# Optimization experiments

Measured on AMD Instinct MI355X. Metric: run time of the kernel, lower is better.

Reference implementation:

```python
import jax, jax.numpy as jnp
import numpy as np

B, S, D_IN, D_OUT = 4, 2048, 1024, 1024

def setup_inputs() -> dict:
    key = jax.random.key(0)
    k1, k2, k3, k4 = jax.random.split(key, 4)
    s = 0.02
    return {
        "X": jax.random.normal(k1, (B, S, D_IN), dtype=jnp.float32),
        "Wq": jax.random.normal(k2, (D_OUT, D_IN), dtype=jnp.float32) * s,
        "Wk": jax.random.normal(k3, (D_OUT, D_IN), dtype=jnp.float32) * s,
        "Wv": jax.random.normal(k4, (D_OUT, D_IN), dtype=jnp.float32) * s,
    }

def reference(X, Wq, Wk, Wv):
    # nn.Linear: y = x @ W.T (no bias)
    q = jnp.einsum('bsd,ed->bse', X, Wq)  # [B,S,D_OUT]
    k = jnp.einsum('bsd,ed->bse', X, Wk)
    v = jnp.einsum('bsd,ed->bse', X, Wv)
    scores = jnp.einsum('bqe,bke->bqk', q, k)  # [B,S,S]
    n = X.shape[1]
    causal = jnp.triu(jnp.ones((n, n), dtype=bool), k=1)
    scores = jnp.where(causal[None], -jnp.inf, scores)
    scale = 1.0 / jnp.sqrt(jnp.asarray(k.shape[-1], dtype=scores.dtype))
    attn = jax.nn.softmax(scores * scale, axis=-1)
    return jnp.einsum('bqk,bke->bqe', attn, v)
```

## Files before the change

kernel.cpp:

```cpp
#include <hip/hip_runtime.h>
#include <cstdint>


typedef __attribute__((ext_vector_type(8))) __bf16 bf16x8;
typedef __attribute__((ext_vector_type(4))) float f32x4;

#define BK 64

__device__ __forceinline__ unsigned short f2bf(float f) {
  union { float f; unsigned u; } v; v.f = f;
  unsigned r = v.u + 0x7fffu + ((v.u >> 16) & 1u);
  return (unsigned short)(r >> 16);
}

__device__ __forceinline__ void gload_lds16(const void* g, void* l) {
  __builtin_amdgcn_global_load_lds(
      (const __attribute__((address_space(1))) void*)g,
      (__attribute__((address_space(3))) void*)l, 16, 0, 0);
}

__global__ __launch_bounds__(256)
void cvt_all(const float* __restrict__ X, const float* __restrict__ Wq,
             const float* __restrict__ Wk, const float* __restrict__ Wv,
             unsigned short* __restrict__ Xbf, unsigned short* __restrict__ Wall,
             float* __restrict__ L) {
  const int bid = blockIdx.x;
  if (bid >= 11264) {
    float4* p = (float4*)(L + (size_t)(bid - 11264) * 2048);
    p[threadIdx.x] = (float4){0.f, 0.f, 0.f, 0.f};
    p[threadIdx.x + 256] = (float4){0.f, 0.f, 0.f, 0.f};
    return;
  }
  const float* src;
  unsigned short* dst;
  int i;
  if (bid < 8192) {
    src = X; dst = Xbf; i = bid * 256 + threadIdx.x;
  } else {
    const int m = bid - 8192;
    const int sel = m >> 10;
    src = (sel == 0) ? Wq : (sel == 1) ? Wk : Wv;
    dst = Wall + (size_t)sel * 1048576;
    i = (m & 1023) * 256 + threadIdx.x;
  }
  float4 v = ((const float4*)src)[i];
  ushort4 o;
  o.x = f2bf(v.x); o.y = f2bf(v.y); o.z = f2bf(v.z); o.w = f2bf(v.w);
  ((ushort4*)dst)[i] = o;
}

__global__ __launch_bounds__(256, 3)
void gemm_qkv(const unsigned short* __restrict__ A,
              const unsigned short* __restrict__ Bm,
              unsigned short* __restrict__ Qb,
              unsigned short* __restrict__ Kb)
{
  const int NX = gridDim.x;
  const int lin = blockIdx.y * NX + blockIdx.x;
  const int chunk = (NX * 64) >> 3;
  const int swz = (lin & 7) * chunk + (lin >> 3);
  const int bx = swz % NX, by = swz / NX;

  __shared__ __align__(16) unsigned short As[128 * BK];
  __shared__ __align__(16) unsigned short Bs[128 * BK];

  const int tid = threadIdx.x;
  const int wave = tid >> 6, lane = tid & 63;
  const int wr = wave >> 1, wc = wave & 1;
  const int quad = lane >> 4, l16 = lane & 15;

  const unsigned rsub = wave * 8 + (lane >> 3);
  const unsigned csb = (unsigned)(((lane & 7) ^ ((lane >> 3) & 7)) * 16);

  unsigned offA[4], offB[4];
  #pragma unroll
  for (int s = 0; s < 4; ++s) {
    offA[s] = ((unsigned)(by * 128 + s * 32 + rsub) * 1024u) * 2u + csb;
    offB[s] = ((unsigned)(bx * 128 + s * 32 + rsub) * 1024u) * 2u + csb;
  }
  const char* Abase = (const char*)A;
  const char* Bbase = (const char*)Bm;

  f32x4 acc[4][4];
  #pragma unroll
  for (int i = 0; i < 4; ++i)
    #pragma unroll
    for (int j = 0; j < 4; ++j)
      acc[i][j] = (f32x4){0.f, 0.f, 0.f, 0.f};

  const int pq = (quad ^ (l16 & 7)) * 8;
  const int aOff = (wr * 64 + l16) * BK + pq;
  const int bOff = (wc * 64 + l16) * BK + pq;

  for (int k0 = 0; k0 < 1024; k0 += BK) {
    const unsigned kb = (unsigned)k0 * 2u;
    #pragma unroll
    for (int s = 0; s < 4; ++s) {
      gload_lds16(Abase + kb + offA[s], As + s * 2048 + wave * 512);
      gload_lds16(Bbase + kb + offB[s], Bs + s * 2048 + wave * 512);
    }
    __syncthreads();
    #pragma unroll
    for (int h = 0; h < 2; ++h) {
      const int hx = h * 32;
      bf16x8 af[4], bfr[4];
      #pragma unroll
      for (int i = 0; i < 4; ++i)
        af[i] = *(const bf16x8*)(As + ((aOff + i * 16 * BK) ^ hx));
      #pragma unroll
      for (int j = 0; j < 4; ++j)
        bfr[j] = *(const bf16x8*)(Bs + ((bOff + j * 16 * BK) ^ hx));
      #pragma unroll
      for (int i = 0; i < 4; ++i)
        #pragma unroll
        for (int j = 0; j < 4; ++j)
          acc[i][j] = __builtin_amdgcn_mfma_f32_16x16x32_bf16(af[i], bfr[j], acc[i][j], 0, 0, 0);
    }
    __syncthreads();
  }

  const int row0 = by * 128 + wr * 64 + quad * 4;
  const int col0 = bx * 128 + wc * 64 + l16;
  unsigned short* C = (bx < 8) ? Qb : Kb;
  const int col = (bx < 8) ? col0 : col0 - 1024;
  #pragma unroll
  for (int i = 0; i < 4; ++i)
    #pragma unroll
    for (int r = 0; r < 4; ++r) {
      const size_t rr = (size_t)(row0 + i * 16 + r) * 1024;
      #pragma unroll
      for (int j = 0; j < 4; ++j)
        C[rr + col + j * 16] = f2bf(acc[i][j][r]);
    }
}

__global__ __launch_bounds__(256, 3)
void gemm_sv(const unsigned short* __restrict__ Qb,
             const unsigned short* __restrict__ Kb,
             const unsigned short* __restrict__ Xbf,
             const unsigned short* __restrict__ Wall,
             unsigned short* __restrict__ S,
             float* __restrict__ L,
             unsigned short* __restrict__ Vt)
{
  const int lin = blockIdx.x;
  const int c = lin & 7;
  const int pos = lin >> 3;
  const bool isV = (pos < 128) && (pos & 1);

  int by, bxr, bz = 0;
  const unsigned short *Ab, *Bb;
  if (!isV) {
    const int s_loc = (pos < 128) ? (pos >> 1) : (64 + (pos - 128));
    const int sidx = c * 68 + s_loc;
    bz = sidx / 136;
    const int t = sidx - bz * 136;
    int byy = (int)((sqrtf(8.f * t + 1.f) - 1.f) * 0.5f);
    while ((byy + 1) * (byy + 2) / 2 <= t) ++byy;
    while (byy * (byy + 1) / 2 > t) --byy;
    by = byy;
    bxr = t - byy * (byy + 1) / 2;
    Ab = Qb + (size_t)bz * 2097152;
    Bb = Kb + (size_t)bz * 2097152;
  } else {
    const int v = c * 64 + (pos >> 1);
    by = v >> 3;
    bxr = v & 7;
    Ab = Xbf;
    Bb = Wall + 2 * 1048576;
  }

  __shared__ __align__(16) unsigned short As2[128 * BK];
  __shared__ __align__(16) unsigned short Bs2[128 * BK];

  const int tid = threadIdx.x;
  const int wave = tid >> 6, lane = tid & 63;
  const int wr = wave >> 1, wc = wave & 1;
  const int quad = lane >> 4, l16 = lane & 15;

  const unsigned rsub = wave * 8 + (lane >> 3);
  const unsigned csb = (unsigned)(((lane & 7) ^ ((lane >> 3) & 7)) * 16);

  unsigned offA[4], offB[4];
  #pragma unroll
  for (int s = 0; s < 4; ++s) {
    offA[s] = ((unsigned)(by * 128 + s * 32 + rsub) * 1024u) * 2u + csb;
    offB[s] = ((unsigned)(bxr * 128 + s * 32 + rsub) * 1024u) * 2u + csb;
  }
  const char* Abase = (const char*)Ab;
  const char* Bbase = (const char*)Bb;

  f32x4 acc[4][4];
  #pragma unroll
  for (int i = 0; i < 4; ++i)
    #pragma unroll
    for (int j = 0; j < 4; ++j)
      acc[i][j] = (f32x4){0.f, 0.f, 0.f, 0.f};

  const int pq = (quad ^ (l16 & 7)) * 8;
  const int aOff = (wr * 64 + l16) * BK + pq;
  const int bOff = (wc * 64 + l16) * BK + pq;

  for (int k0 = 0; k0 < 1024; k0 += BK) {
    const unsigned kb = (unsigned)k0 * 2u;
    #pragma unroll
    for (int s = 0; s < 4; ++s) {
      gload_lds16(Abase + kb + offA[s], As2 + s * 2048 + wave * 512);
      gload_lds16(Bbase + kb + offB[s], Bs2 + s * 2048 + wave * 512);
    }
    __syncthreads();
    #pragma unroll
    for (int h = 0; h < 2; ++h) {
      const int hx = h * 32;
      bf16x8 af[4], bfr[4];
      #pragma unroll
      for (int i = 0; i < 4; ++i)
        af[i] = *(const bf16x8*)(As2 + ((aOff + i * 16 * BK) ^ hx));
      #pragma unroll
      for (int j = 0; j < 4; ++j)
        bfr[j] = *(const bf16x8*)(Bs2 + ((bOff + j * 16 * BK) ^ hx));
      #pragma unroll
      for (int i = 0; i < 4; ++i)
        #pragma unroll
        for (int j = 0; j < 4; ++j)
          acc[i][j] = __builtin_amdgcn_mfma_f32_16x16x32_bf16(af[i], bfr[j], acc[i][j], 0, 0, 0);
    }
    __syncthreads();
  }

  const int row0 = by * 128 + wr * 64 + quad * 4;
  if (!isV) {
    const int col0 = bxr * 128 + wc * 64 + l16;
    float* Lb = L + (size_t)bz * 2048;
    unsigned short* C = S + (size_t)bz * 4194304;
    #pragma unroll
    for (int i = 0; i < 4; ++i)
      #pragma unroll
      for (int r = 0; r < 4; ++r) {
        const int grow = row0 + i * 16 + r;
        float ps = 0.f;
        #pragma unroll
        for (int j = 0; j < 4; ++j) {
          const int gcol = col0 + j * 16;
          float e = (gcol <= grow) ? __expf(acc[i][j][r] * 0.03125f) : 0.f;
          acc[i][j][r] = e;
          ps += e;
        }
        #pragma unroll
        for (int m = 8; m > 0; m >>= 1)
          ps += __shfl_xor(ps, m);
        if (l16 == 0) atomicAdd(&Lb[grow], ps);
        const size_t rr = (size_t)grow * 2048;
        #pragma unroll
        for (int j = 0; j < 4; ++j)
          C[rr + col0 + j * 16] = f2bf(acc[i][j][r]);
      }
  } else {
    const int b = row0 >> 11;
    const int s0 = row0 & 2047;
    unsigned short* Vb = Vt + (size_t)b * 2097152;
    const int e0 = bxr * 128 + wc * 64 + l16;
    #pragma unroll
    for (int j = 0; j < 4; ++j) {
      const size_t ee = (size_t)(e0 + j * 16) * 2048;
      #pragma unroll
      for (int i = 0; i < 4; ++i) {
        ushort4 o;
        o.x = f2bf(acc[i][j][0]); o.y = f2bf(acc[i][j][1]);
        o.z = f2bf(acc[i][j][2]); o.w = f2bf(acc[i][j][3]);
        *(ushort4*)(Vb + ee + s0 + i * 16) = o;
      }
    }
  }
}

__global__ __launch_bounds__(256, 3)
void gemm_pv(const unsigned short* __restrict__ P,
             const unsigned short* __restrict__ Vt,
             float* __restrict__ Out,
             const float* __restrict__ L)
{
  const int bx = blockIdx.x, by = 15 - blockIdx.y, bz = blockIdx.z;

  __shared__ __align__(16) unsigned short As2[128 * BK];
  __shared__ __align__(16) unsigned short Bs2[128 * BK];

  const int tid = threadIdx.x;
  const int wave = tid >> 6, lane = tid & 63;
  const int wr = wave >> 1, wc = wave & 1;
  const int quad = lane >> 4, l16 = lane & 15;

  const unsigned rsub = wave * 8 + (lane >> 3);
  const unsigned csb = (unsigned)(((lane & 7) ^ ((lane >> 3) & 7)) * 16);

  unsigned offA[4], offB[4];
  #pragma unroll
  for (int s = 0; s < 4; ++s) {
    offA[s] = ((unsigned)(by * 128 + s * 32 + rsub) * 2048u) * 2u + csb;
    offB[s] = ((unsigned)(bx * 128 + s * 32 + rsub) * 2048u) * 2u + csb;
  }
  const char* Abase = (const char*)(P + (size_t)bz * 4194304);
  const char* Bbase = (const char*)(Vt + (size_t)bz * 2097152);

  f32x4 acc[4][4];
  #pragma unroll
  for (int i = 0; i < 4; ++i)
    #pragma unroll
    for (int j = 0; j < 4; ++j)
      acc[i][j] = (f32x4){0.f, 0.f, 0.f, 0.f};

  const int kmax = (by + 1) * 128;

  const int pq = (quad ^ (l16 & 7)) * 8;
  const int aOff = (wr * 64 + l16) * BK + pq;
  const int bOff = (wc * 64 + l16) * BK + pq;

  for (int k0 = 0; k0 < kmax; k0 += BK) {
    const unsigned kb = (unsigned)k0 * 2u;
    #pragma unroll
    for (int s = 0; s < 4; ++s) {
      gload_lds16(Abase + kb + offA[s], As2 + s * 2048 + wave * 512);
      gload_lds16(Bbase + kb + offB[s], Bs2 + s * 2048 + wave * 512);
    }
    __syncthreads();
    #pragma unroll
    for (int h = 0; h < 2; ++h) {
      const int hx = h * 32;
      bf16x8 af[4], bfr[4];
      #pragma unroll
      for (int i = 0; i < 4; ++i)
        af[i] = *(const bf16x8*)(As2 + ((aOff + i * 16 * BK) ^ hx));
      #pragma unroll
      for (int j = 0; j < 4; ++j)
        bfr[j] = *(const bf16x8*)(Bs2 + ((bOff + j * 16 * BK) ^ hx));
      #pragma unroll
      for (int i = 0; i < 4; ++i)
        #pragma unroll
        for (int j = 0; j < 4; ++j)
          acc[i][j] = __builtin_amdgcn_mfma_f32_16x16x32_bf16(af[i], bfr[j], acc[i][j], 0, 0, 0);
    }
    __syncthreads();
  }

  const int row0 = by * 128 + wr * 64 + quad * 4;
  const int col0 = bx * 128 + wc * 64 + l16;
  float* C = Out + (size_t)bz * 2097152;
  const float* Lb = L + (size_t)bz * 2048;
  #pragma unroll
  for (int i = 0; i < 4; ++i)
    #pragma unroll
    for (int r = 0; r < 4; ++r) {
      const int grow = row0 + i * 16 + r;
      const float inv = 1.0f / Lb[grow];
      const size_t rr = (size_t)grow * 1024;
      #pragma unroll
      for (int j = 0; j < 4; ++j)
        C[rr + col0 + j * 16] = acc[i][j][r] * inv;
    }
}

extern "C" void kernel_launch(void* const* d_in, const int* in_sizes, int n_in,
                              void* d_out, int out_size, void* d_ws, size_t ws_size,
                              hipStream_t stream) {
  const float* X  = (const float*)d_in[0];
  const float* Wq = (const float*)d_in[1];
  const float* Wk = (const float*)d_in[2];
  const float* Wv = (const float*)d_in[3];
  float* Out = (float*)d_out;

  char* ws = (char*)d_ws;
  unsigned short* Xbf  = (unsigned short*)(ws);
  unsigned short* Wall = (unsigned short*)(ws + 16777216);
  unsigned short* Qbf  = (unsigned short*)(ws + 23068672);
  unsigned short* Kbf  = (unsigned short*)(ws + 39845888);
  unsigned short* Vt   = (unsigned short*)(ws + 56623104);
  unsigned short* Sbf  = (unsigned short*)(ws + 73400320);
  float*          Lbuf = (float*)(ws + 106954752);

  cvt_all<<<11268, 256, 0, stream>>>(X, Wq, Wk, Wv, Xbf, Wall, Lbuf);

  gemm_qkv<<<dim3(16, 64), 256, 0, stream>>>(Xbf, Wall, Qbf, Kbf);

  gemm_sv<<<1056, 256, 0, stream>>>(Qbf, Kbf, Xbf, Wall, Sbf, Lbuf, Vt);

  gemm_pv<<<dim3(8, 16, 4), 256, 0, stream>>>(Sbf, Vt, Out, Lbuf);
}
```

Before: 218.0 us.

## Split-K the long causal row blocks in PV GEMM with atomic accumulation

The PV GEMM now splits the K range of the bottom half of row blocks (by 8-15, the longest causal rows) into two halves handled by separate blocks, which accumulate into the output with atomicAdd. The output rows for those blocks are zeroed in the conversion kernel beforehand. The aim is to balance the triangular workload and shorten the tail of the grid, at the cost of an extra zeroing pass over half of the output and slower atomic stores for those tiles.

```diff
diff --git a/kernel.cpp b/kernel.cpp
--- a/kernel.cpp
+++ b/kernel.cpp
@@ -23,8 +23,17 @@
 void cvt_all(const float* __restrict__ X, const float* __restrict__ Wq,
              const float* __restrict__ Wk, const float* __restrict__ Wv,
              unsigned short* __restrict__ Xbf, unsigned short* __restrict__ Wall,
-             float* __restrict__ L) {
+             float* __restrict__ L, float* __restrict__ Out) {
   const int bid = blockIdx.x;
+  if (bid >= 11268) {
+    const int m = bid - 11268;
+    const int bz = m >> 8, blk = m & 255;
+    float4* p = (float4*)(Out + (size_t)bz * 2097152 + 1048576 + (size_t)blk * 4096);
+    #pragma unroll
+    for (int u = 0; u < 4; ++u)
+      p[threadIdx.x + u * 256] = (float4){0.f, 0.f, 0.f, 0.f};
+    return;
+  }
   if (bid >= 11264) {
     float4* p = (float4*)(L + (size_t)(bid - 11264) * 2048);
     p[threadIdx.x] = (float4){0.f, 0.f, 0.f, 0.f};
@@ -280,7 +289,20 @@
              float* __restrict__ Out,
              const float* __restrict__ L)
 {
-  const int bx = blockIdx.x, by = 15 - blockIdx.y, bz = blockIdx.z;
+  const int bx = blockIdx.x, bz = blockIdx.z;
+  const bool split = (blockIdx.y < 16);
+  int by, kbeg, kend;
+  if (split) {
+    by = 8 + (blockIdx.y >> 1);
+    const int half = blockIdx.y & 1;
+    const int hlen = (by + 1) * 64;
+    kbeg = half * hlen;
+    kend = kbeg + hlen;
+  } else {
+    by = 23 - blockIdx.y;
+    kbeg = 0;
+    kend = (by + 1) * 128;
+  }
 
   __shared__ __align__(16) unsigned short As2[128 * BK];
   __shared__ __align__(16) unsigned short Bs2[128 * BK];
@@ -309,13 +331,11 @@
     for (int j = 0; j < 4; ++j)
       acc[i][j] = (f32x4){0.f, 0.f, 0.f, 0.f};
 
-  const int kmax = (by + 1) * 128;
-
   const int pq = (quad ^ (l16 & 7)) * 8;
   const int aOff = (wr * 64 + l16) * BK + pq;
   const int bOff = (wc * 64 + l16) * BK + pq;
 
-  for (int k0 = 0; k0 < kmax; k0 += BK) {
+  for (int k0 = kbeg; k0 < kend; k0 += BK) {
     const unsigned kb = (unsigned)k0 * 2u;
     #pragma unroll
     for (int s = 0; s < 4; ++s) {
@@ -346,17 +366,31 @@
   const int col0 = bx * 128 + wc * 64 + l16;
   float* C = Out + (size_t)bz * 2097152;
   const float* Lb = L + (size_t)bz * 2048;
-  #pragma unroll
-  for (int i = 0; i < 4; ++i)
-    #pragma unroll
-    for (int r = 0; r < 4; ++r) {
-      const int grow = row0 + i * 16 + r;
-      const float inv = 1.0f / Lb[grow];
-      const size_t rr = (size_t)grow * 1024;
-      #pragma unroll
-      for (int j = 0; j < 4; ++j)
-        C[rr + col0 + j * 16] = acc[i][j][r] * inv;
-    }
+  if (split) {
+    #pragma unroll
+    for (int i = 0; i < 4; ++i)
+      #pragma unroll
+      for (int r = 0; r < 4; ++r) {
+        const int grow = row0 + i * 16 + r;
+        const float inv = 1.0f / Lb[grow];
+        const size_t rr = (size_t)grow * 1024;
+        #pragma unroll
+        for (int j = 0; j < 4; ++j)
+          atomicAdd(&C[rr + col0 + j * 16], acc[i][j][r] * inv);
+      }
+  } else {
+    #pragma unroll
+    for (int i = 0; i < 4; ++i)
+      #pragma unroll
+      for (int r = 0; r < 4; ++r) {
+        const int grow = row0 + i * 16 + r;
+        const float inv = 1.0f / Lb[grow];
+        const size_t rr = (size_t)grow * 1024;
+        #pragma unroll
+        for (int j = 0; j < 4; ++j)
+          C[rr + col0 + j * 16] = acc[i][j][r] * inv;
+      }
+  }
 }
 
 extern "C" void kernel_launch(void* const* d_in, const int* in_sizes, int n_in,
@@ -377,11 +411,11 @@
   unsigned short* Sbf  = (unsigned short*)(ws + 73400320);
   float*          Lbuf = (float*)(ws + 106954752);
 
-  cvt_all<<<11268, 256, 0, stream>>>(X, Wq, Wk, Wv, Xbf, Wall, Lbuf);
+  cvt_all<<<12292, 256, 0, stream>>>(X, Wq, Wk, Wv, Xbf, Wall, Lbuf, Out);
 
   gemm_qkv<<<dim3(16, 64), 256, 0, stream>>>(Xbf, Wall, Qbf, Kbf);
 
   gemm_sv<<<1056, 256, 0, stream>>>(Qbf, Kbf, Xbf, Wall, Sbf, Lbuf, Vt);
 
-  gemm_pv<<<dim3(8, 16, 4), 256, 0, stream>>>(Sbf, Vt, Out, Lbuf);
-}
+  gemm_pv<<<dim3(8, 24, 4), 256, 0, stream>>>(Sbf, Vt, Out, Lbuf);
+}
```

Result: slower. 227.4 us (+4.3%).
